# Kernel tuning notes

Measured on AMD Instinct MI355X. Metric: run time of the kernel, lower is better.

The kernel has to match this reference:

```python
import jax, jax.numpy as jnp
import numpy as np

N, E, F, H, L = 100000, 1200000, 64, 64, 4


def setup_inputs() -> dict:
    key = jax.random.key(0)
    ks = jax.random.split(key, 24)
    s = 1.0 / np.sqrt(H)
    x = jax.random.normal(ks[0], (N, F), dtype=jnp.float32)
    edge_index = jax.random.randint(ks[1], (2, E), 0, N, dtype=jnp.int32)
    W1 = jax.random.normal(ks[2], (F, H), jnp.float32) / np.sqrt(F)
    b1 = jnp.zeros((H,), jnp.float32)
    W2 = jax.random.normal(ks[3], (H, H), jnp.float32) * s
    b2 = jnp.zeros((H,), jnp.float32)
    # stacked per-direction (2: fw, bw) per-layer (L) conv params
    def mk(k):
        return jax.random.normal(k, (2, L, H, H), jnp.float32) * s
    gWk, gWq, gWv, gWs = mk(ks[4]), mk(ks[5]), mk(ks[6]), mk(ks[7])
    gbk = jnp.zeros((2, L, H), jnp.float32)
    gbq = jnp.zeros((2, L, H), jnp.float32)
    gbv = jnp.zeros((2, L, H), jnp.float32)
    gb = jnp.zeros((2, L, H), jnp.float32)
    Wsc = jax.random.normal(ks[8], (2 * H, 1), jnp.float32) / np.sqrt(2 * H)
    bsc = jnp.zeros((1,), jnp.float32)
    return dict(x=x, edge_index=edge_index, W1=W1, b1=b1, W2=W2, b2=b2,
                gWk=gWk, gbk=gbk, gWq=gWq, gbq=gbq, gWv=gWv, gbv=gbv,
                gWs=gWs, gb=gb, Wsc=Wsc, bsc=bsc)


def _res_gated_conv(h, src, dst, Wk, bk, Wq, bq, Wv, bv, Ws, b):
    # PyG ResGatedGraphConv: out_i = h_i @ Ws + b + sum_{(j->i)} sigmoid(k_i + q_j) * v_j
    k = h @ Wk + bk            # [N,H]
    q = h @ Wq + bq            # [N,H]
    v = h @ Wv + bv            # [N,H]
    eta = jax.nn.sigmoid(k[dst] + q[src])          # [E,H] per-edge gate
    agg = jax.ops.segment_sum(eta * v[src], dst, num_segments=h.shape[0])
    return agg + h @ Ws + b


def reference(x, edge_index, W1, b1, W2, b2, gWk, gbk, gWq, gbq, gWv, gbv, gWs, gb, Wsc, bsc):
    h = jax.nn.relu(x @ W1 + b1) @ W2 + b2
    src, dst = edge_index[0], edge_index[1]
    # forward direction: messages source -> target (aggregate at dst)
    h_fw = h
    for l in range(L):
        h_fw = _res_gated_conv(h_fw, src, dst, gWk[0, l], gbk[0, l], gWq[0, l], gbq[0, l],
                               gWv[0, l], gbv[0, l], gWs[0, l], gb[0, l])
    # backward direction: flow 'target_to_source' (aggregate at src)
    h_bw = h
    for l in range(L):
        h_bw = _res_gated_conv(h_bw, dst, src, gWk[1, l], gbk[1, l], gWq[1, l], gbq[1, l],
                               gWv[1, l], gbv[1, l], gWs[1, l], gb[1, l])
    score = jnp.concatenate([h_fw, h_bw], axis=1) @ Wsc + bsc
    return score
```

## Files before the change

kernel.cpp:

```cpp
#include <hip/hip_runtime.h>
#include <hip/hip_bf16.h>
#include <hip/hip_fp16.h>


constexpr int HDIM = 64;
constexpr int CAP = 42;
constexpr int NBIN = 2 * (CAP + 1);
constexpr int RANGE = 128;
constexpr int RSHIFT = 7;
constexpr int BLD_BLOCKS = 512;

union H2U { uint32_t u; __half2 h2; };
union H1U { unsigned short u; __half h; };

typedef _Float16 f16x2 __attribute__((ext_vector_type(2)));
union F2U { uint32_t u; f16x2 h; };

__device__ __forceinline__ float fdot2(f16x2 a, f16x2 b, float c) {
#if __has_builtin(__builtin_amdgcn_fdot2)
    return __builtin_amdgcn_fdot2(a, b, c, false);
#else
    return fmaf((float)a.x, (float)b.x, fmaf((float)a.y, (float)b.y, c));
#endif
}

__global__ __launch_bounds__(256) void mlp_kernel(
    const float* __restrict__ x, const float* __restrict__ W1, const float* __restrict__ b1,
    const float* __restrict__ W2, const float* __restrict__ b2,
    float* __restrict__ hfw, float* __restrict__ hbw, int N, int ntiles)
{
    __shared__ float sW1[64 * 64];
    __shared__ float sW2[64 * 64];
    __shared__ float sb1[64], sb2[64];
    __shared__ float sh[64][36];
    int t = threadIdx.x;
    for (int i = t; i < 1024; i += 256) {
        ((float4*)sW1)[i] = ((const float4*)W1)[i];
        ((float4*)sW2)[i] = ((const float4*)W2)[i];
    }
    if (t < 64) { sb1[t] = b1[t]; sb2[t] = b2[t]; }
    int c = t & 63, rg = t >> 6;

    for (int tile = blockIdx.x; tile < ntiles; tile += gridDim.x) {
        int base = tile * 32;
        __syncthreads();
        for (int i = t; i < 32 * 16; i += 256) {
            int r = i >> 4, fq = i & 15;
            int row = base + r;
            float4 hv = make_float4(0.f, 0.f, 0.f, 0.f);
            if (row < N) hv = ((const float4*)x)[(size_t)row * 16 + fq];
            sh[fq * 4 + 0][r] = hv.x; sh[fq * 4 + 1][r] = hv.y;
            sh[fq * 4 + 2][r] = hv.z; sh[fq * 4 + 3][r] = hv.w;
        }
        __syncthreads();

        float acc[8];
        #pragma unroll
        for (int r = 0; r < 8; r++) acc[r] = sb1[c];
        #pragma unroll 4
        for (int f = 0; f < 64; f++) {
            float w = sW1[f * 64 + c];
            float4 ha = *(const float4*)&sh[f][rg * 8];
            float4 hb = *(const float4*)&sh[f][rg * 8 + 4];
            float hr[8] = {ha.x, ha.y, ha.z, ha.w, hb.x, hb.y, hb.z, hb.w};
            #pragma unroll
            for (int r = 0; r < 8; r++) acc[r] = fmaf(hr[r], w, acc[r]);
        }
        __syncthreads();
        #pragma unroll
        for (int r = 0; r < 8; r++) sh[c][rg * 8 + r] = fmaxf(acc[r], 0.f);
        __syncthreads();

        float acc2[8];
        #pragma unroll
        for (int r = 0; r < 8; r++) acc2[r] = sb2[c];
        #pragma unroll 4
        for (int f = 0; f < 64; f++) {
            float w = sW2[f * 64 + c];
            float4 ha = *(const float4*)&sh[f][rg * 8];
            float4 hb = *(const float4*)&sh[f][rg * 8 + 4];
            float hr[8] = {ha.x, ha.y, ha.z, ha.w, hb.x, hb.y, hb.z, hb.w};
            #pragma unroll
            for (int r = 0; r < 8; r++) acc2[r] = fmaf(hr[r], w, acc2[r]);
        }
        #pragma unroll
        for (int r = 0; r < 8; r++) {
            int row = base + rg * 8 + r;
            if (row < N) {
                hfw[(size_t)row * 64 + c] = acc2[r];
                hbw[(size_t)row * 64 + c] = acc2[r];
            }
        }
    }
}

__global__ __launch_bounds__(256) void bexp_count(
    const int* __restrict__ srcA, const int* __restrict__ dstA,
    int* __restrict__ gcount, int* __restrict__ blockBase, int E, int NR)
{
    extern __shared__ int hist[];
    int nb2 = 2 * NR;
    for (int i = threadIdx.x; i < nb2; i += 256) hist[i] = 0;
    __syncthreads();
    int stride = gridDim.x * 256;
    for (int e = blockIdx.x * 256 + threadIdx.x; e < E; e += stride) {
        int s = srcA[e], d = dstA[e];
        atomicAdd(&hist[d >> RSHIFT], 1);
        atomicAdd(&hist[NR + (s >> RSHIFT)], 1);
    }
    __syncthreads();
    for (int i = threadIdx.x; i < nb2; i += 256) {
        int c = hist[i];
        blockBase[(size_t)blockIdx.x * nb2 + i] = c ? atomicAdd(&gcount[i], c) : 0;
    }
}

__global__ __launch_bounds__(256) void bexp_scan(
    const int* __restrict__ gcount, int* __restrict__ bucketBase, int nb2)
{
    __shared__ int ssum[256];
    int t = threadIdx.x;
    constexpr int PER = 8;
    int base = t * PER;
    int loc[PER];
    int s = 0;
    #pragma unroll
    for (int k = 0; k < PER; k++) {
        int idx = base + k;
        int v = (idx < nb2) ? gcount[idx] : 0;
        loc[k] = s;
        s += v;
    }
    ssum[t] = s;
    __syncthreads();
    #pragma unroll
    for (int off = 1; off < 256; off <<= 1) {
        int tmp = (t >= off) ? ssum[t - off] : 0;
        __syncthreads();
        ssum[t] += tmp;
        __syncthreads();
    }
    int prefix = (t > 0) ? ssum[t - 1] : 0;
    #pragma unroll
    for (int k = 0; k < PER; k++) {
        int idx = base + k;
        if (idx < nb2) bucketBase[idx] = prefix + loc[k];
    }
}

__global__ __launch_bounds__(256) void bexp_scatter(
    const int* __restrict__ srcA, const int* __restrict__ dstA,
    const int* __restrict__ bucketBase, const int* __restrict__ blockBase,
    uint2* __restrict__ bucket, int E, int NR)
{
    extern __shared__ int cur[];
    int nb2 = 2 * NR;
    for (int i = threadIdx.x; i < nb2; i += 256) cur[i] = 0;
    __syncthreads();
    int stride = gridDim.x * 256;
    const int* bb = blockBase + (size_t)blockIdx.x * nb2;
    for (int e = blockIdx.x * 256 + threadIdx.x; e < E; e += stride) {
        int s = srcA[e], d = dstA[e];
        int bf = d >> RSHIFT;
        int r = atomicAdd(&cur[bf], 1);
        bucket[bucketBase[bf] + bb[bf] + r] = make_uint2((unsigned)d, (unsigned)s);
        int bw = NR + (s >> RSHIFT);
        int r2 = atomicAdd(&cur[bw], 1);
        bucket[bucketBase[bw] + bb[bw] + r2] = make_uint2((unsigned)s, (unsigned)d);
    }
}

__global__ __launch_bounds__(256) void bexp_fill(
    const uint2* __restrict__ bucket, const int* __restrict__ gcount,
    const int* __restrict__ bucketBase,
    int* __restrict__ col_fw, int* __restrict__ col_bw,
    int* __restrict__ deg_fw, int* __restrict__ deg_bw, int N, int NR)
{
    __shared__ int cnt[RANGE];
    __shared__ int win[RANGE * CAP];
    int blk = blockIdx.x;
    int dir = blk >= NR;
    int r = dir ? blk - NR : blk;
    int lo = r * RANGE;
    int nnode = min(RANGE, N - lo);
    if (nnode <= 0) return;
    for (int i = threadIdx.x; i < RANGE; i += 256) cnt[i] = 0;
    __syncthreads();
    int base = bucketBase[blk], tot = gcount[blk];
    for (int i = threadIdx.x; i < tot; i += 256) {
        uint2 en = bucket[base + i];
        int li = (int)en.x - lo;
        int c = atomicAdd(&cnt[li], 1);
        if (c < CAP) win[li * CAP + c] = (int)en.y;
    }
    __syncthreads();
    int* col = dir ? col_bw : col_fw;
    int* deg = dir ? deg_bw : deg_fw;
    int total = nnode * CAP;
    for (int i = threadIdx.x; i < total; i += 256) col[(size_t)lo * CAP + i] = win[i];
    for (int i = threadIdx.x; i < nnode; i += 256) deg[lo + i] = cnt[i];
}

__global__ __launch_bounds__(256) void dsort_phase1(
    const int* __restrict__ deg_fw, const int* __restrict__ deg_bw,
    int* __restrict__ gcount, int* __restrict__ blockBase, int N)
{
    __shared__ int hist[NBIN];
    int t = threadIdx.x;
    if (t < NBIN) hist[t] = 0;
    __syncthreads();
    int i = blockIdx.x * 256 + t;
    if (i < N) {
        atomicAdd(&hist[min(deg_fw[i], CAP)], 1);
        atomicAdd(&hist[(CAP + 1) + min(deg_bw[i], CAP)], 1);
    }
    __syncthreads();
    if (t < NBIN) {
        int c = hist[t];
        int old = c ? atomicAdd(&gcount[t], c) : 0;
        blockBase[(size_t)blockIdx.x * NBIN + t] = old;
    }
}

__global__ __launch_bounds__(64) void dsort_phase2(
    const int* __restrict__ gcount, int* __restrict__ bucketBase)
{
    int base = blockIdx.x * (CAP + 1);
    int t = threadIdx.x;
    int v = (t <= CAP) ? gcount[base + t] : 0;
    int s = v;
    #pragma unroll
    for (int off = 1; off < 64; off <<= 1) {
        int u = __shfl_up(s, off, 64);
        if (t >= off) s += u;
    }
    if (t <= CAP) bucketBase[base + t] = s - v;
}

__global__ __launch_bounds__(256) void dsort_phase3(
    const int* __restrict__ deg_fw, const int* __restrict__ deg_bw,
    const int* __restrict__ bucketBase, const int* __restrict__ blockBase,
    int* __restrict__ perm_fw, int* __restrict__ perm_bw, int N)
{
    __shared__ int cur[NBIN];
    int t = threadIdx.x;
    if (t < NBIN) cur[t] = 0;
    __syncthreads();
    int i = blockIdx.x * 256 + t;
    if (i < N) {
        int bf = min(deg_fw[i], CAP);
        int r = atomicAdd(&cur[bf], 1);
        perm_fw[bucketBase[bf] + blockBase[(size_t)blockIdx.x * NBIN + bf] + r] = i;
        int bb = (CAP + 1) + min(deg_bw[i], CAP);
        int r2 = atomicAdd(&cur[bb], 1);
        perm_bw[bucketBase[bb] + blockBase[(size_t)blockIdx.x * NBIN + bb] + r2] = i;
    }
}

__global__ __launch_bounds__(256) void kqvs_kernel(
    const float* h,
    const float* __restrict__ Wk, const float* __restrict__ bk,
    const float* __restrict__ Wq, const float* __restrict__ bq,
    const float* __restrict__ Wv, const float* __restrict__ bv,
    const float* __restrict__ Ws, const float* __restrict__ bs,
    unsigned short* __restrict__ ko, uint32_t* __restrict__ qvo,
    float* oo, int N, int ntiles)
{
    __shared__ f16x2 sW[4][32 * 64];
    __shared__ float sb[4][64];
    __shared__ f16x2 sh[32][34];
    int t = threadIdx.x;
    {
        const float* Wsrc[4] = {Wk, Wq, Wv, Ws};
        #pragma unroll
        for (int m = 0; m < 4; m++) {
            const float* W = Wsrc[m];
            for (int i = t; i < 512; i += 256) {
                int fp = i >> 4, cq = (i & 15) * 4;
                float4 wa = *(const float4*)&W[(size_t)(2 * fp) * 64 + cq];
                float4 wb = *(const float4*)&W[(size_t)(2 * fp + 1) * 64 + cq];
                f16x2 p0 = {(_Float16)wa.x, (_Float16)wb.x};
                f16x2 p1 = {(_Float16)wa.y, (_Float16)wb.y};
                f16x2 p2 = {(_Float16)wa.z, (_Float16)wb.z};
                f16x2 p3 = {(_Float16)wa.w, (_Float16)wb.w};
                sW[m][fp * 64 + cq + 0] = p0;
                sW[m][fp * 64 + cq + 1] = p1;
                sW[m][fp * 64 + cq + 2] = p2;
                sW[m][fp * 64 + cq + 3] = p3;
            }
        }
        if (t < 64) { sb[0][t] = bk[t]; sb[1][t] = bq[t]; sb[2][t] = bv[t]; sb[3][t] = bs[t]; }
    }
    int c = t & 63, rg = t >> 6;

    for (int tile = blockIdx.x; tile < ntiles; tile += gridDim.x) {
        int base = tile * 32;
        __syncthreads();
        for (int i = t; i < 32 * 16; i += 256) {
            int r = i >> 4, fq = i & 15;
            int row = base + r;
            float4 hv = make_float4(0.f, 0.f, 0.f, 0.f);
            if (row < N) hv = ((const float4*)h)[(size_t)row * 16 + fq];
            f16x2 pa = {(_Float16)hv.x, (_Float16)hv.y};
            f16x2 pb = {(_Float16)hv.z, (_Float16)hv.w};
            sh[fq * 2 + 0][r] = pa;
            sh[fq * 2 + 1][r] = pb;
        }
        __syncthreads();

        float acc[8][4];
        #pragma unroll
        for (int r = 0; r < 8; r++) {
            acc[r][0] = sb[0][c]; acc[r][1] = sb[1][c]; acc[r][2] = sb[2][c]; acc[r][3] = sb[3][c];
        }
        #pragma unroll 4
        for (int fp = 0; fp < 32; fp++) {
            f16x2 w0 = sW[0][fp * 64 + c], w1 = sW[1][fp * 64 + c];
            f16x2 w2 = sW[2][fp * 64 + c], w3 = sW[3][fp * 64 + c];
            uint4 A = *(const uint4*)&sh[fp][rg * 8];
            uint4 B = *(const uint4*)&sh[fp][rg * 8 + 4];
            uint32_t hw[8] = {A.x, A.y, A.z, A.w, B.x, B.y, B.z, B.w};
            #pragma unroll
            for (int r = 0; r < 8; r++) {
                F2U hr; hr.u = hw[r];
                acc[r][0] = fdot2(hr.h, w0, acc[r][0]);
                acc[r][1] = fdot2(hr.h, w1, acc[r][1]);
                acc[r][2] = fdot2(hr.h, w2, acc[r][2]);
                acc[r][3] = fdot2(hr.h, w3, acc[r][3]);
            }
        }
        #pragma unroll
        for (int r = 0; r < 8; r++) {
            int row = base + rg * 8 + r;
            if (row < N) {
                size_t o = (size_t)row * 64 + c;
                H1U pk1; pk1.h = __float2half_rn(acc[r][0]);
                ko[o] = pk1.u;
                H2U pk;
                pk.h2.x = __float2half_rn(acc[r][1]);
                pk.h2.y = __float2half_rn(acc[r][2]);
                qvo[o] = pk.u;
                oo[o] = acc[r][3];
            }
        }
    }
}

__device__ __forceinline__ float gate_eta(float kd, uint32_t u, float* vf) {
    H2U c; c.u = u;
    float qf = __low2float(c.h2);
    *vf = __high2float(c.h2);
    return __builtin_amdgcn_rcpf(1.f + __expf(-(kd + qf)));
}

__global__ __launch_bounds__(256) void edge_csr_kernel(
    const int* __restrict__ perm, const int* __restrict__ deg,
    const int* __restrict__ col,
    const uint2* __restrict__ kh2, const uint4* __restrict__ qv4,
    float* h, const float* __restrict__ hother,
    const float* __restrict__ Wsc, const float* __restrict__ bsc,
    float* __restrict__ outp, int do_score, int N)
{
    int t = threadIdx.x;
    int l = t & 15;
    int qd = (t >> 4) & 3;
    int w = (blockIdx.x * 256 + t) >> 6;
    int nw = (gridDim.x * 256) >> 6;
    int nquads = (N + 3) >> 2;
    for (int p = w; p < nquads; p += nw) {
        int task = p * 4 + qd;
        bool act = task < N;
        int i = act ? perm[task] : 0;
        int dg = act ? min(deg[i], CAP) : 0;
        int j = i * CAP, je = j + dg;
        size_t o = (size_t)i * 16 + l;
        uint2 ku = kh2[o];
        H2U k0, k1; k0.u = ku.x; k1.u = ku.y;
        float kd0 = __low2float(k0.h2), kd1 = __high2float(k0.h2);
        float kd2 = __low2float(k1.h2), kd3 = __high2float(k1.h2);
        float4 hold = ((const float4*)h)[o];
        float a0 = 0.f, a1 = 0.f, a2 = 0.f, a3 = 0.f;
        #define GT4(U) { float v0,v1,v2,v3; \
                         float e0 = gate_eta(kd0, (U).x, &v0); \
                         float e1 = gate_eta(kd1, (U).y, &v1); \
                         float e2 = gate_eta(kd2, (U).z, &v2); \
                         float e3 = gate_eta(kd3, (U).w, &v3); \
                         a0 = fmaf(e0, v0, a0); a1 = fmaf(e1, v1, a1); \
                         a2 = fmaf(e2, v2, a2); a3 = fmaf(e3, v3, a3); }
        while (j + 8 <= je) {
            int s0 = col[j + 0], s1 = col[j + 1], s2 = col[j + 2], s3 = col[j + 3];
            int s4 = col[j + 4], s5 = col[j + 5], s6 = col[j + 6], s7 = col[j + 7];
            uint4 u0 = qv4[(size_t)s0 * 16 + l];
            uint4 u1 = qv4[(size_t)s1 * 16 + l];
            uint4 u2 = qv4[(size_t)s2 * 16 + l];
            uint4 u3 = qv4[(size_t)s3 * 16 + l];
            uint4 u4 = qv4[(size_t)s4 * 16 + l];
            uint4 u5 = qv4[(size_t)s5 * 16 + l];
            uint4 u6 = qv4[(size_t)s6 * 16 + l];
            uint4 u7 = qv4[(size_t)s7 * 16 + l];
            GT4(u0); GT4(u1); GT4(u2); GT4(u3);
            GT4(u4); GT4(u5); GT4(u6); GT4(u7);
            j += 8;
        }
        if (j + 4 <= je) {
            int s0 = col[j + 0], s1 = col[j + 1], s2 = col[j + 2], s3 = col[j + 3];
            uint4 u0 = qv4[(size_t)s0 * 16 + l];
            uint4 u1 = qv4[(size_t)s1 * 16 + l];
            uint4 u2 = qv4[(size_t)s2 * 16 + l];
            uint4 u3 = qv4[(size_t)s3 * 16 + l];
            GT4(u0); GT4(u1); GT4(u2); GT4(u3);
            j += 4;
        }
        while (j < je) {
            int s0 = col[j];
            uint4 u0 = qv4[(size_t)s0 * 16 + l];
            GT4(u0);
            ++j;
        }
        #undef GT4
        float4 nh = make_float4(a0 + hold.x, a1 + hold.y, a2 + hold.z, a3 + hold.w);
        if (act) ((float4*)h)[o] = nh;
        if (do_score) {
            float4 hf = make_float4(0.f, 0.f, 0.f, 0.f);
            if (act) hf = ((const float4*)hother)[o];
            const float4 wf = ((const float4*)Wsc)[l];
            const float4 wb = ((const float4*)Wsc)[16 + l];
            float pp = hf.x * wf.x + hf.y * wf.y + hf.z * wf.z + hf.w * wf.w
                     + nh.x * wb.x + nh.y * wb.y + nh.z * wb.z + nh.w * wb.w;
            #pragma unroll
            for (int off = 8; off; off >>= 1) pp += __shfl_xor(pp, off, 64);
            if (act && l == 0) outp[i] = pp + bsc[0];
        }
    }
}

extern "C" void kernel_launch(void* const* d_in, const int* in_sizes, int n_in,
                              void* d_out, int out_size, void* d_ws, size_t ws_size,
                              hipStream_t stream)
{
    const float* x   = (const float*)d_in[0];
    const int*   ei  = (const int*)d_in[1];
    const float* W1  = (const float*)d_in[2];
    const float* b1  = (const float*)d_in[3];
    const float* W2  = (const float*)d_in[4];
    const float* b2  = (const float*)d_in[5];
    const float* gWk = (const float*)d_in[6];
    const float* gbk = (const float*)d_in[7];
    const float* gWq = (const float*)d_in[8];
    const float* gbq = (const float*)d_in[9];
    const float* gWv = (const float*)d_in[10];
    const float* gbv = (const float*)d_in[11];
    const float* gWs = (const float*)d_in[12];
    const float* gb  = (const float*)d_in[13];
    const float* Wsc = (const float*)d_in[14];
    const float* bsc = (const float*)d_in[15];

    const int N = in_sizes[0] / HDIM;
    const int E = in_sizes[1] / 2;
    const int L = 4;
    const int NR = (N + RANGE - 1) / RANGE;
    const int nb2 = 2 * NR;
    int nb = (N + 255) / 256;
    int ntiles = (N + 31) / 32;

    size_t N64 = (size_t)N * HDIM;
    size_t Npad = (size_t)N + 64;
    float* ws    = (float*)d_ws;
    float* h_fw  = ws;
    float* h_bw  = ws + N64;
    uint32_t* qvbuf = (uint32_t*)(ws + 2 * N64);
    unsigned short* kbuf = (unsigned short*)(ws + 3 * N64);
    int* deg_fw  = (int*)(ws + 3 * N64 + N64 / 2);
    int* deg_bw  = deg_fw + Npad;
    int* gcountE = deg_bw + Npad;
    int* bucketBaseE = gcountE + 2048;
    int* gcountD = bucketBaseE + 2048;
    int* bucketBaseD = gcountD + 128;
    int* blockBase = bucketBaseD + 128;
    int* perm_fw = blockBase + (size_t)BLD_BLOCKS * 2048;
    int* perm_bw = perm_fw + N;
    int* col_fw  = perm_bw + N;
    int* col_bw  = col_fw + (size_t)N * CAP;
    uint2* bucket = (uint2*)qvbuf;

    const int* srcA = ei;
    const int* dstA = ei + E;

    mlp_kernel<<<768, 256, 0, stream>>>(x, W1, b1, W2, b2, h_fw, h_bw, N, ntiles);

    hipMemsetAsync(gcountE, 0, (2048 + 2048 + 128 + 128) * sizeof(int), stream);
    bexp_count<<<BLD_BLOCKS, 256, nb2 * sizeof(int), stream>>>(srcA, dstA, gcountE, blockBase, E, NR);
    bexp_scan<<<1, 256, 0, stream>>>(gcountE, bucketBaseE, nb2);
    bexp_scatter<<<BLD_BLOCKS, 256, nb2 * sizeof(int), stream>>>(srcA, dstA, bucketBaseE, blockBase,
                                                                 bucket, E, NR);
    bexp_fill<<<nb2, 256, 0, stream>>>(bucket, gcountE, bucketBaseE,
                                       col_fw, col_bw, deg_fw, deg_bw, N, NR);

    dsort_phase1<<<nb, 256, 0, stream>>>(deg_fw, deg_bw, gcountD, blockBase, N);
    dsort_phase2<<<2, 64, 0, stream>>>(gcountD, bucketBaseD);
    dsort_phase3<<<nb, 256, 0, stream>>>(deg_fw, deg_bw, bucketBaseD, blockBase,
                                         perm_fw, perm_bw, N);

    for (int dir = 0; dir < 2; dir++) {
        float* h = dir ? h_bw : h_fw;
        float* hother = dir ? h_fw : h_bw;
        const int* perm = dir ? perm_bw : perm_fw;
        const int* deg  = dir ? deg_bw : deg_fw;
        const int* col  = dir ? col_bw : col_fw;
        for (int l = 0; l < L; l++) {
            int off = dir * L + l;
            int do_score = (dir == 1 && l == L - 1) ? 1 : 0;
            kqvs_kernel<<<1024, 256, 0, stream>>>(h,
                gWk + (size_t)off * 4096, gbk + (size_t)off * 64,
                gWq + (size_t)off * 4096, gbq + (size_t)off * 64,
                gWv + (size_t)off * 4096, gbv + (size_t)off * 64,
                gWs + (size_t)off * 4096, gb  + (size_t)off * 64,
                kbuf, qvbuf, h, N, ntiles);
            edge_csr_kernel<<<2048, 256, 0, stream>>>(perm, deg, col,
                (const uint2*)kbuf, (const uint4*)qvbuf, h, hother,
                Wsc, bsc, (float*)d_out, do_score, N);
        }
    }
}
```

Measured before the change: 881.3 us.

## Batch fw/bw directions per layer and store hidden state in fp16

Runs the forward and backward GNN directions together, one kqvs and one edge kernel per layer, with blocks or warps split by direction. This halves the number of launches and exposes more parallelism per launch. Hidden states h_fw/h_bw are now kept as packed fp16 instead of fp32, which halves the bytes read and written for the residual and the projection input. The final score moves into a separate kernel. The cost is fp16 precision on the residual stream across layers and duplicated k/qv buffers.

Measured after the change: 842.7 us. 1.05x faster.

```diff
diff --git a/kernel.cpp b/kernel.cpp
--- a/kernel.cpp
+++ b/kernel.cpp
@@ -24,10 +24,14 @@
 #endif
 }
 
+__device__ __forceinline__ uint32_t pack_h2(float lo, float hi) {
+    H2U p; p.h2 = __floats2half2_rn(lo, hi); return p.u;
+}
+
 __global__ __launch_bounds__(256) void mlp_kernel(
     const float* __restrict__ x, const float* __restrict__ W1, const float* __restrict__ b1,
     const float* __restrict__ W2, const float* __restrict__ b2,
-    float* __restrict__ hfw, float* __restrict__ hbw, int N, int ntiles)
+    uint32_t* __restrict__ hfw, uint32_t* __restrict__ hbw, int N, int ntiles)
 {
     __shared__ float sW1[64 * 64];
     __shared__ float sW2[64 * 64];
@@ -85,10 +89,12 @@
         }
         #pragma unroll
         for (int r = 0; r < 8; r++) {
+            float prt = __shfl_xor(acc2[r], 1, 64);
             int row = base + rg * 8 + r;
-            if (row < N) {
-                hfw[(size_t)row * 64 + c] = acc2[r];
-                hbw[(size_t)row * 64 + c] = acc2[r];
+            if (!(c & 1) && row < N) {
+                uint32_t pw = pack_h2(acc2[r], prt);
+                hfw[(size_t)row * 32 + (c >> 1)] = pw;
+                hbw[(size_t)row * 32 + (c >> 1)] = pw;
             }
         }
     }
@@ -257,19 +263,30 @@
     }
 }
 
-__global__ __launch_bounds__(256) void kqvs_kernel(
-    const float* h,
-    const float* __restrict__ Wk, const float* __restrict__ bk,
-    const float* __restrict__ Wq, const float* __restrict__ bq,
-    const float* __restrict__ Wv, const float* __restrict__ bv,
-    const float* __restrict__ Ws, const float* __restrict__ bs,
-    unsigned short* __restrict__ ko, uint32_t* __restrict__ qvo,
-    float* oo, int N, int ntiles)
+__global__ __launch_bounds__(256) void kqvs_both(
+    uint32_t* hA, uint32_t* hB,
+    const float* __restrict__ gWk, const float* __restrict__ gbk,
+    const float* __restrict__ gWq, const float* __restrict__ gbq,
+    const float* __restrict__ gWv, const float* __restrict__ gbv,
+    const float* __restrict__ gWs, const float* __restrict__ gb,
+    unsigned short* __restrict__ kA, unsigned short* __restrict__ kB,
+    uint32_t* __restrict__ qvA, uint32_t* __restrict__ qvB,
+    int l, int N, int ntiles, int halfGrid)
 {
     __shared__ f16x2 sW[4][32 * 64];
     __shared__ float sb[4][64];
-    __shared__ f16x2 sh[32][34];
-    int t = threadIdx.x;
+    __shared__ uint32_t shu[32][34];
+    int t = threadIdx.x;
+    int dir = blockIdx.x >= halfGrid;
+    int brank = dir ? blockIdx.x - halfGrid : blockIdx.x;
+    uint32_t* h = dir ? hB : hA;
+    unsigned short* ko = dir ? kB : kA;
+    uint32_t* qvo = dir ? qvB : qvA;
+    size_t off = (size_t)(dir * 4 + l);
+    const float* Wk = gWk + off * 4096; const float* bk = gbk + off * 64;
+    const float* Wq = gWq + off * 4096; const float* bq = gbq + off * 64;
+    const float* Wv = gWv + off * 4096; const float* bv = gbv + off * 64;
+    const float* Ws = gWs + off * 4096; const float* bs = gb  + off * 64;
     {
         const float* Wsrc[4] = {Wk, Wq, Wv, Ws};
         #pragma unroll
@@ -293,18 +310,16 @@
     }
     int c = t & 63, rg = t >> 6;
 
-    for (int tile = blockIdx.x; tile < ntiles; tile += gridDim.x) {
+    for (int tile = brank; tile < ntiles; tile += halfGrid) {
         int base = tile * 32;
         __syncthreads();
-        for (int i = t; i < 32 * 16; i += 256) {
-            int r = i >> 4, fq = i & 15;
+        {
+            int r = t >> 3, g = t & 7;
             int row = base + r;
-            float4 hv = make_float4(0.f, 0.f, 0.f, 0.f);
-            if (row < N) hv = ((const float4*)h)[(size_t)row * 16 + fq];
-            f16x2 pa = {(_Float16)hv.x, (_Float16)hv.y};
-            f16x2 pb = {(_Float16)hv.z, (_Float16)hv.w};
-            sh[fq * 2 + 0][r] = pa;
-            sh[fq * 2 + 1][r] = pb;
+            uint4 hv = make_uint4(0u, 0u, 0u, 0u);
+            if (row < N) hv = ((const uint4*)h)[(size_t)row * 8 + g];
+            shu[g * 4 + 0][r] = hv.x; shu[g * 4 + 1][r] = hv.y;
+            shu[g * 4 + 2][r] = hv.z; shu[g * 4 + 3][r] = hv.w;
         }
         __syncthreads();
 
@@ -317,8 +332,8 @@
         for (int fp = 0; fp < 32; fp++) {
             f16x2 w0 = sW[0][fp * 64 + c], w1 = sW[1][fp * 64 + c];
             f16x2 w2 = sW[2][fp * 64 + c], w3 = sW[3][fp * 64 + c];
-            uint4 A = *(const uint4*)&sh[fp][rg * 8];
-            uint4 B = *(const uint4*)&sh[fp][rg * 8 + 4];
+            uint4 A = *(const uint4*)&shu[fp][rg * 8];
+            uint4 B = *(const uint4*)&shu[fp][rg * 8 + 4];
             uint32_t hw[8] = {A.x, A.y, A.z, A.w, B.x, B.y, B.z, B.w};
             #pragma unroll
             for (int r = 0; r < 8; r++) {
@@ -332,6 +347,7 @@
         #pragma unroll
         for (int r = 0; r < 8; r++) {
             int row = base + rg * 8 + r;
+            float prt = __shfl_xor(acc[r][3], 1, 64);
             if (row < N) {
                 size_t o = (size_t)row * 64 + c;
                 H1U pk1; pk1.h = __float2half_rn(acc[r][0]);
@@ -340,7 +356,7 @@
                 pk.h2.x = __float2half_rn(acc[r][1]);
                 pk.h2.y = __float2half_rn(acc[r][2]);
                 qvo[o] = pk.u;
-                oo[o] = acc[r][3];
+                if (!(c & 1)) h[(size_t)row * 32 + (c >> 1)] = pack_h2(acc[r][3], prt);
             }
         }
     }
@@ -353,32 +369,43 @@
     return __builtin_amdgcn_rcpf(1.f + __expf(-(kd + qf)));
 }
 
-__global__ __launch_bounds__(256) void edge_csr_kernel(
-    const int* __restrict__ perm, const int* __restrict__ deg,
-    const int* __restrict__ col,
-    const uint2* __restrict__ kh2, const uint4* __restrict__ qv4,
-    float* h, const float* __restrict__ hother,
-    const float* __restrict__ Wsc, const float* __restrict__ bsc,
-    float* __restrict__ outp, int do_score, int N)
+__global__ __launch_bounds__(256) void edge_both(
+    const int* __restrict__ permA, const int* __restrict__ permB,
+    const int* __restrict__ degA, const int* __restrict__ degB,
+    const int* __restrict__ colA, const int* __restrict__ colB,
+    const uint2* __restrict__ kA2, const uint2* __restrict__ kB2,
+    const uint4* __restrict__ qvA4, const uint4* __restrict__ qvB4,
+    uint32_t* hA, uint32_t* hB, int N)
 {
     int t = threadIdx.x;
     int l = t & 15;
     int qd = (t >> 4) & 3;
     int w = (blockIdx.x * 256 + t) >> 6;
     int nw = (gridDim.x * 256) >> 6;
-    int nquads = (N + 3) >> 2;
-    for (int p = w; p < nquads; p += nw) {
-        int task = p * 4 + qd;
+    int nqN = (N + 3) >> 2;
+    for (int p = w; p < 2 * nqN; p += nw) {
+        int dir = p >= nqN;
+        int pl = dir ? p - nqN : p;
+        const int* perm = dir ? permB : permA;
+        const int* deg  = dir ? degB : degA;
+        const int* col  = dir ? colB : colA;
+        const uint2* kh2 = dir ? kB2 : kA2;
+        const uint4* qv4 = dir ? qvB4 : qvA4;
+        uint32_t* h = dir ? hB : hA;
+
+        int task = pl * 4 + qd;
         bool act = task < N;
         int i = act ? perm[task] : 0;
         int dg = act ? min(deg[i], CAP) : 0;
         int j = i * CAP, je = j + dg;
-        size_t o = (size_t)i * 16 + l;
-        uint2 ku = kh2[o];
+        uint2 ku = kh2[(size_t)i * 16 + l];
         H2U k0, k1; k0.u = ku.x; k1.u = ku.y;
         float kd0 = __low2float(k0.h2), kd1 = __high2float(k0.h2);
         float kd2 = __low2float(k1.h2), kd3 = __high2float(k1.h2);
-        float4 hold = ((const float4*)h)[o];
+        uint2 hp = ((const uint2*)h)[(size_t)i * 16 + l];
+        H2U hx, hy; hx.u = hp.x; hy.u = hp.y;
+        float h0 = __low2float(hx.h2), h1 = __high2float(hx.h2);
+        float h2v = __low2float(hy.h2), h3 = __high2float(hy.h2);
         float a0 = 0.f, a1 = 0.f, a2 = 0.f, a3 = 0.f;
         #define GT4(U) { float v0,v1,v2,v3; \
                          float e0 = gate_eta(kd0, (U).x, &v0); \
@@ -418,19 +445,34 @@
             ++j;
         }
         #undef GT4
-        float4 nh = make_float4(a0 + hold.x, a1 + hold.y, a2 + hold.z, a3 + hold.w);
-        if (act) ((float4*)h)[o] = nh;
-        if (do_score) {
-            float4 hf = make_float4(0.f, 0.f, 0.f, 0.f);
-            if (act) hf = ((const float4*)hother)[o];
-            const float4 wf = ((const float4*)Wsc)[l];
-            const float4 wb = ((const float4*)Wsc)[16 + l];
-            float pp = hf.x * wf.x + hf.y * wf.y + hf.z * wf.z + hf.w * wf.w
-                     + nh.x * wb.x + nh.y * wb.y + nh.z * wb.z + nh.w * wb.w;
-            #pragma unroll
-            for (int off = 8; off; off >>= 1) pp += __shfl_xor(pp, off, 64);
-            if (act && l == 0) outp[i] = pp + bsc[0];
-        }
+        if (act) {
+            uint2 op;
+            op.x = pack_h2(a0 + h0, a1 + h1);
+            op.y = pack_h2(a2 + h2v, a3 + h3);
+            ((uint2*)h)[(size_t)i * 16 + l] = op;
+        }
+    }
+}
+
+__global__ __launch_bounds__(256) void score_kernel(
+    const uint32_t* __restrict__ hfw, const uint32_t* __restrict__ hbw,
+    const float* __restrict__ Wsc, const float* __restrict__ bsc,
+    float* __restrict__ outv, int N)
+{
+    int t = threadIdx.x;
+    int lane = t & 63;
+    int half = lane >> 5, li = lane & 31;
+    int wid = (blockIdx.x * 256 + t) >> 6;
+    int nw = (gridDim.x * 256) >> 6;
+    float w0 = Wsc[half * 64 + 2 * li], w1 = Wsc[half * 64 + 2 * li + 1];
+    float b = bsc[0];
+    for (int r = wid; r < N; r += nw) {
+        uint32_t u = half ? hbw[(size_t)r * 32 + li] : hfw[(size_t)r * 32 + li];
+        H2U c; c.u = u;
+        float p = __low2float(c.h2) * w0 + __high2float(c.h2) * w1;
+        #pragma unroll
+        for (int off = 32; off; off >>= 1) p += __shfl_xor(p, off, 64);
+        if (lane == 0) outv[r] = p + b;
     }
 }
 
@@ -463,14 +505,16 @@
     int nb = (N + 255) / 256;
     int ntiles = (N + 31) / 32;
 
-    size_t N64 = (size_t)N * HDIM;
+    size_t N32 = (size_t)N * 32;
     size_t Npad = (size_t)N + 64;
-    float* ws    = (float*)d_ws;
-    float* h_fw  = ws;
-    float* h_bw  = ws + N64;
-    uint32_t* qvbuf = (uint32_t*)(ws + 2 * N64);
-    unsigned short* kbuf = (unsigned short*)(ws + 3 * N64);
-    int* deg_fw  = (int*)(ws + 3 * N64 + N64 / 2);
+    uint32_t* wsu = (uint32_t*)d_ws;
+    uint32_t* h_fw = wsu;
+    uint32_t* h_bw = h_fw + N32;
+    uint32_t* qv_fw = h_bw + N32;
+    uint32_t* qv_bw = qv_fw + 2 * N32;
+    unsigned short* k_fw = (unsigned short*)(qv_bw + 2 * N32);
+    unsigned short* k_bw = k_fw + (size_t)N * 64;
+    int* deg_fw  = (int*)(k_bw + (size_t)N * 64);
     int* deg_bw  = deg_fw + Npad;
     int* gcountE = deg_bw + Npad;
     int* bucketBaseE = gcountE + 2048;
@@ -481,7 +525,7 @@
     int* perm_bw = perm_fw + N;
     int* col_fw  = perm_bw + N;
     int* col_bw  = col_fw + (size_t)N * CAP;
-    uint2* bucket = (uint2*)qvbuf;
+    uint2* bucket = (uint2*)qv_fw;
 
     const int* srcA = ei;
     const int* dstA = ei + E;
@@ -501,24 +545,14 @@
     dsort_phase3<<<nb, 256, 0, stream>>>(deg_fw, deg_bw, bucketBaseD, blockBase,
                                          perm_fw, perm_bw, N);
 
-    for (int dir = 0; dir < 2; dir++) {
-        float* h = dir ? h_bw : h_fw;
-        float* hother = dir ? h_fw : h_bw;
-        const int* perm = dir ? perm_bw : perm_fw;
-        const int* deg  = dir ? deg_bw : deg_fw;
-        const int* col  = dir ? col_bw : col_fw;
-        for (int l = 0; l < L; l++) {
-            int off = dir * L + l;
-            int do_score = (dir == 1 && l == L - 1) ? 1 : 0;
-            kqvs_kernel<<<1024, 256, 0, stream>>>(h,
-                gWk + (size_t)off * 4096, gbk + (size_t)off * 64,
-                gWq + (size_t)off * 4096, gbq + (size_t)off * 64,
-                gWv + (size_t)off * 4096, gbv + (size_t)off * 64,
-                gWs + (size_t)off * 4096, gb  + (size_t)off * 64,
-                kbuf, qvbuf, h, N, ntiles);
-            edge_csr_kernel<<<2048, 256, 0, stream>>>(perm, deg, col,
-                (const uint2*)kbuf, (const uint4*)qvbuf, h, hother,
-                Wsc, bsc, (float*)d_out, do_score, N);
-        }
-    }
-}
+    for (int l = 0; l < L; l++) {
+        kqvs_both<<<1024, 256, 0, stream>>>(h_fw, h_bw,
+            gWk, gbk, gWq, gbq, gWv, gbv, gWs, gb,
+            k_fw, k_bw, qv_fw, qv_bw, l, N, ntiles, 512);
+        edge_both<<<4096, 256, 0, stream>>>(perm_fw, perm_bw, deg_fw, deg_bw,
+            col_fw, col_bw, (const uint2*)k_fw, (const uint2*)k_bw,
+            (const uint4*)qv_fw, (const uint4*)qv_bw, h_fw, h_bw, N);
+    }
+
+    score_kernel<<<1024, 256, 0, stream>>>(h_fw, h_bw, Wsc, bsc, (float*)d_out, N);
+}
```
